# Performance work log

Hardware: AMD Instinct MI355X
Metric: run time of the kernel (lower is better)

Reference implementation:

```python
import jax, jax.numpy as jnp
import numpy as np

B = 4; IN_CH = 256; HEAD_CH = 64; NUM_CLS = 3; H = 128; W = 128
NH = 4; KEY = 16; VAL = 16; OUT_CH = 2
VX = 0.1 * 8; VY = 0.1 * 8  # voxel_size[:2] * out_size_factor
DW = 1.6; DL = 3.9; STRIDE = 1
C_CTR = (HEAD_CH + 2 + NUM_CLS) * 9      # 621
C_COR = (HEAD_CH + 2 + NUM_CLS * 4) * 8  # 624
C_FG = (HEAD_CH + 2 + NUM_CLS) * 9       # 621


def _sampler_points():
    offs = np.arange(-STRIDE, STRIDE + 1, STRIDE, dtype=np.float32)
    oy, ox = np.meshgrid(offs, offs, indexing='ij')
    ctr = np.stack([ox, oy], 0).reshape(2, 9)  # pixel offsets
    cx = np.array([-DW/2, -DW/2, DW/2, DW/2, DL/2, -DL/2, DL/2, -DL/2], np.float32) / VX
    cy = np.array([DL/2, -DL/2, DL/2, -DL/2, -DW/2, -DW/2, DW/2, DW/2], np.float32) / VY
    # faithful to torch: stack(dim=1) -> [8,2] then .view(2,8) (row-major reinterpret)
    cor = np.stack([cx, cy], 1).reshape(2, 8)
    r = max(DW, DL)
    fx = np.array([-r/3, -r/3, -r/3, 0, 0, 0, r/3, r/3, r/3], np.float32) / VX
    fy = np.array([-r/3, 0, r/3, -r/3, 0, r/3, -r/3, 0, r/3], np.float32) / VY
    fg = np.stack([fx, fy], 1).reshape(2, 9)
    return jnp.asarray(ctr), jnp.asarray(cor), jnp.asarray(fg)


def _raw_grid():
    gx = jnp.arange(W, dtype=jnp.float32) + 0.5
    gy = jnp.arange(H, dtype=jnp.float32) + 0.5
    return jnp.stack([jnp.broadcast_to(gx[None, :], (H, W)),
                      jnp.broadcast_to(gy[:, None], (H, W))], 0)  # [2,H,W]


def _conv3x3(x, w, b):
    y = jax.lax.conv_general_dilated(x, w, (1, 1), 'SAME',
                                     dimension_numbers=('NCHW', 'OIHW', 'NCHW'))
    return y + b[None, :, None, None]


def _cbr3(x, w, b, s, t):  # conv3x3 + inference-mode BN (folded scale/shift) + relu
    return jax.nn.relu(_conv3x3(x, w, b) * s[None, :, None, None] + t[None, :, None, None])


def _cbr1(x, w, b, s, t):  # per-head 1x1 conv + BN + relu, w: [NH,O,C], x: [B,C,H,W]
    y = jnp.einsum('noc,bchw->nbohw', w, x) + b[:, None, :, None, None]
    return jax.nn.relu(y * s[:, None, :, None, None] + t[:, None, :, None, None])


def _sample(feats, grids):
    # feats [B,C,H,W]; grids [2,n,H,W] pixel coords. Matches F.grid_sample
    # (bilinear, zeros padding, align_corners=False): sample at pixel coord g-0.5.
    n = grids.shape[1]
    geo = jnp.stack([grids[0] / W, grids[1] / H], 0)  # recover_coords, [2,n,H,W]
    gx, gy = grids[0] - 0.5, grids[1] - 0.5
    x0f = jnp.floor(gx); y0f = jnp.floor(gy)
    dx, dy = gx - x0f, gy - y0f
    x0 = x0f.astype(jnp.int32); y0 = y0f.astype(jnp.int32)
    flat = feats.reshape(B, -1, H * W)

    def gather(xc, yc, wgt):
        valid = ((xc >= 0) & (xc < W) & (yc >= 0) & (yc < H)).astype(feats.dtype) * wgt
        idx = jnp.clip(yc, 0, H - 1) * W + jnp.clip(xc, 0, W - 1)
        v = jnp.take(flat, idx.reshape(-1), axis=2).reshape(B, -1, n, H, W)
        return v * valid[None, None]

    s = (gather(x0, y0, (1 - dx) * (1 - dy)) + gather(x0 + 1, y0, dx * (1 - dy))
         + gather(x0, y0 + 1, (1 - dx) * dy) + gather(x0 + 1, y0 + 1, dx * dy))
    geo_b = jnp.broadcast_to(geo[None], (B,) + geo.shape)
    out = jnp.concatenate([s, geo_b], axis=1)  # [B,C+2,n,H,W]
    return out.reshape(B, -1, H, W)           # channel index = c*n + p, as torch .view


def _forward(base_feats, cc_w, cc_b, cc_s, cc_t, ch_w, ch_b,
             oc_w, oc_b, oc_s, oc_t, oh_w, oh_b,
             fc_w, fc_b, fc_s, fc_t, fh_w, fh_b,
             q_w, q_b, q_s, q_t,
             ck_w, ck_b, ck_s, ck_t, cv_w, cv_b, cv_s, cv_t,
             kk_w, kk_b, kk_s, kk_t, kv_w, kv_b, kv_s, kv_t,
             fk_w, fk_b, fk_s, fk_t, fv_w, fv_b, fv_s, fv_t,
             p1_w, p1_b, p1_s, p1_t, p2_w, p2_b):
    center_feat = _cbr3(base_feats, cc_w, cc_b, cc_s, cc_t)
    center_map = _conv3x3(center_feat, ch_w, ch_b)
    corner_feat = _cbr3(base_feats, oc_w, oc_b, oc_s, oc_t)
    corner_map = _conv3x3(corner_feat, oh_w, oh_b)
    fg_feat = _cbr3(base_feats, fc_w, fc_b, fc_s, fc_t)
    fg_map = _conv3x3(fg_feat, fh_w, fh_b)

    ctr_pts, cor_pts, fg_pts = _sampler_points()
    raw = _raw_grid()
    g_ctr = raw[:, None] + ctr_pts[:, :, None, None]  # [2,9,H,W]
    g_cor = raw[:, None] + cor_pts[:, :, None, None]  # [2,8,H,W]
    g_fg = raw[:, None] + fg_pts[:, :, None, None]    # [2,9,H,W]

    cs = _sample(jnp.concatenate([center_feat, center_map], 1), g_ctr)  # [B,621,H,W]
    os_ = _sample(jnp.concatenate([corner_feat, corner_map], 1), g_cor)  # [B,624,H,W]
    fs = _sample(jnp.concatenate([fg_feat, fg_map], 1), g_fg)            # [B,621,H,W]

    q = _cbr1(base_feats, q_w, q_b, q_s, q_t)  # [NH,B,KEY,H,W]
    ck = _cbr1(cs, ck_w, ck_b, ck_s, ck_t); cv = _cbr1(cs, cv_w, cv_b, cv_s, cv_t)
    ok = _cbr1(os_, kk_w, kk_b, kk_s, kk_t); ov = _cbr1(os_, kv_w, kv_b, kv_s, kv_t)
    fk = _cbr1(fs, fk_w, fk_b, fk_s, fk_t); fv = _cbr1(fs, fv_w, fv_b, fv_s, fv_t)

    logits = jnp.stack([(q * ck).sum(2), (q * ok).sum(2), (q * fk).sum(2)], axis=2)  # [NH,B,3,H,W]
    attw = jax.nn.softmax(logits, axis=2)
    vals = jnp.stack([cv, ov, fv], axis=2)          # [NH,B,3,VAL,H,W]
    att = (attw[:, :, :, None] * vals).sum(2)       # [NH,B,VAL,H,W]

    # predict: 1x1 conv over cat([base_feats, att]) + BN + relu, then 1x1 to out_ch
    h1 = (jnp.einsum('noc,bchw->nbohw', p1_w[:, :, :IN_CH], base_feats)
          + jnp.einsum('nov,nbvhw->nbohw', p1_w[:, :, IN_CH:], att)
          + p1_b[:, None, :, None, None])
    h1 = jax.nn.relu(h1 * p1_s[:, None, :, None, None] + p1_t[:, None, :, None, None])
    pred = jnp.einsum('npo,nbohw->nbphw', p2_w, h1) + p2_b[:, None, :, None, None]
    heads = jnp.moveaxis(pred, 0, 1).reshape(B, NH * OUT_CH, H, W)
    return jnp.concatenate([center_map, corner_map, fg_map, heads], axis=1)  # [B,26,H,W]


def setup_inputs() -> dict:
    ks = iter(jax.random.split(jax.random.key(0), 80))

    def rn(shape, s=0.05):
        return jax.random.normal(next(ks), shape, jnp.float32) * s

    d = {"base_feats": jax.random.normal(next(ks), (B, IN_CH, H, W), jnp.float32)}
    for conv, head, hc in (("cc", "ch", NUM_CLS), ("oc", "oh", NUM_CLS * 4), ("fc", "fh", NUM_CLS)):
        d[conv + "_w"] = rn((HEAD_CH, IN_CH, 3, 3)); d[conv + "_b"] = rn((HEAD_CH,))
        d[conv + "_s"] = 1.0 + rn((HEAD_CH,)); d[conv + "_t"] = rn((HEAD_CH,))
        d[head + "_w"] = rn((hc, HEAD_CH, 3, 3)); d[head + "_b"] = jnp.full((hc,), -2.19, jnp.float32)
    d["q_w"] = rn((NH, KEY, IN_CH)); d["q_b"] = rn((NH, KEY))
    d["q_s"] = 1.0 + rn((NH, KEY)); d["q_t"] = rn((NH, KEY))
    for name, cin, cout in (("ck", C_CTR, KEY), ("cv", C_CTR, VAL), ("kk", C_COR, KEY),
                            ("kv", C_COR, VAL), ("fk", C_FG, KEY), ("fv", C_FG, VAL)):
        d[name + "_w"] = rn((NH, cout, cin)); d[name + "_b"] = rn((NH, cout))
        d[name + "_s"] = 1.0 + rn((NH, cout)); d[name + "_t"] = rn((NH, cout))
    d["p1_w"] = rn((NH, HEAD_CH, IN_CH + VAL)); d["p1_b"] = rn((NH, HEAD_CH))
    d["p1_s"] = 1.0 + rn((NH, HEAD_CH)); d["p1_t"] = rn((NH, HEAD_CH))
    d["p2_w"] = rn((NH, OUT_CH, HEAD_CH)); d["p2_b"] = jnp.full((NH, OUT_CH), -2.19, jnp.float32)
    return d


def reference(base_feats, cc_w, cc_b, cc_s, cc_t, ch_w, ch_b,
              oc_w, oc_b, oc_s, oc_t, oh_w, oh_b,
              fc_w, fc_b, fc_s, fc_t, fh_w, fh_b,
              q_w, q_b, q_s, q_t,
              ck_w, ck_b, ck_s, ck_t, cv_w, cv_b, cv_s, cv_t,
              kk_w, kk_b, kk_s, kk_t, kv_w, kv_b, kv_s, kv_t,
              fk_w, fk_b, fk_s, fk_t, fv_w, fv_b, fv_s, fv_t,
              p1_w, p1_b, p1_s, p1_t, p2_w, p2_b):
    return _forward(base_feats, cc_w, cc_b, cc_s, cc_t, ch_w, ch_b,
                    oc_w, oc_b, oc_s, oc_t, oh_w, oh_b,
                    fc_w, fc_b, fc_s, fc_t, fh_w, fh_b,
                    q_w, q_b, q_s, q_t,
                    ck_w, ck_b, ck_s, ck_t, cv_w, cv_b, cv_s, cv_t,
                    kk_w, kk_b, kk_s, kk_t, kv_w, kv_b, kv_s, kv_t,
                    fk_w, fk_b, fk_s, fk_t, fv_w, fv_b, fv_s, fv_t,
                    p1_w, p1_b, p1_s, p1_t, p2_w, p2_b)
```

## Files before the change

### kernel.cpp

```cpp
#include <hip/hip_runtime.h>
#include <hip/hip_bf16.h>
#include <math.h>


#define HW 16384
#define WIMG 128

typedef unsigned short ushortT;
typedef __attribute__((ext_vector_type(8))) short short8;
typedef __attribute__((ext_vector_type(4))) float floatx4;

constexpr size_t OFF_KV    = 16777216;
constexpr size_t OFF_A16   = 29360128;
constexpr size_t OFF_B16   = 38012928;
constexpr size_t OFF_CWT   = 46057216;
constexpr size_t OFF_CB    = OFF_CWT + 442368;
constexpr size_t OFF_HWT   = OFF_CB + 192;
constexpr size_t OFF_QWT   = OFF_HWT + 20736;
constexpr size_t OFF_QB    = OFF_QWT + 16384;
constexpr size_t OFF_KVW   = OFF_QB + 64;
constexpr size_t OFF_GEO   = OFF_KVW + 241664;
constexpr size_t OFF_P1WT  = OFF_GEO + 1152;
constexpr size_t OFF_P1B   = OFF_P1WT + 81920;

struct P53 { const float* p[53]; };

__device__ inline ushortT f2bf(float f) {
    unsigned u = __float_as_uint(f);
    unsigned r = (u + 0x7FFFu + ((u >> 16) & 1u)) >> 16;
    return (ushortT)r;
}
__device__ inline unsigned packbf(float a, float b) {
    return (unsigned)f2bf(a) | ((unsigned)f2bf(b) << 16);
}
__device__ inline float bf2f(ushortT u) {
    return __uint_as_float((unsigned)u << 16);
}

__device__ const float c_ox[3][9] = {
    {-1.f, 0.f, 1.f, -1.f, 0.f, 1.f, -1.f, 0.f, 1.f},
    {-1.f, 2.4375f, -1.f, -2.4375f, 1.f, 2.4375f, 1.f, -2.4375f, 0.f},
    {-1.625f, -1.625f, -1.625f, 0.f, -1.625f, 1.625f, 0.f, -1.625f, 0.f}};
__device__ const float c_oy[3][9] = {
    {-1.f, -1.f, -1.f, 0.f, 0.f, 0.f, 1.f, 1.f, 1.f},
    {2.4375f, -1.f, -2.4375f, -1.f, 2.4375f, 1.f, -2.4375f, 1.f, 0.f},
    {0.f, 0.f, 1.625f, 1.625f, -1.625f, 1.625f, 0.f, 1.625f, 1.625f}};

__device__ const int tapX_cor[16] = {-1,-1, 2, 3,-1,-1,-3,-2, 1, 1, 2, 3, 1, 1,-3,-2};
__device__ const int tapY_cor[16] = { 2, 3,-1,-1,-3,-2,-1,-1, 2, 3, 1, 1,-3,-2, 1, 1};
__device__ const int tapR_cor[16] = { 4, 5, 2, 2, 0, 1, 2, 2, 4, 5, 3, 3, 0, 1, 3, 3};

__device__ inline float cornw(float off, int X) {
    float f = floorf(off);
    float d = off - f;
    int fi = (int)f;
    return (X == fi) ? (1.f - d) : (X == fi + 1) ? d : 0.f;
}

__global__ __launch_bounds__(256) void prep_kernel(P53 ptrs, float* __restrict__ ws) {
    int i = blockIdx.x * 256 + threadIdx.x;
    const float* const* p = ptrs.p;
    if (i < 442368) {
        int tap = i / 49152, r = i % 49152;
        int g = r / 1536, r2 = r % 1536;
        int M = r2 >> 3, j = r2 & 7;
        int br = M >> 6, oc = M & 63, ic = g * 8 + j;
        float v = p[1 + 6 * br][(oc * 256 + ic) * 9 + tap] * p[3 + 6 * br][oc];
        ((ushortT*)(ws + OFF_CWT))[i] = f2bf(v);
        return;
    }
    i -= 442368;
    if (i < 192) {
        int br = i >> 6, oc = i & 63;
        ws[OFF_CB + i] = p[2 + 6 * br][oc] * p[3 + 6 * br][oc] + p[4 + 6 * br][oc];
        return;
    }
    i -= 192;
    if (i < 27648) {
        int j = i & 7, m = (i >> 3) & 15, u = (i >> 7) % 72, br = i / 9216;
        int cnt = (br == 1) ? 12 : 3;
        int t = u >> 3, g = u & 7, ic = g * 8 + j;
        const float* hw = (br == 0) ? p[5] : (br == 1) ? p[11] : p[17];
        float v = (m < cnt) ? hw[(m * 64 + ic) * 9 + t] : 0.f;
        ((ushortT*)(ws + OFF_HWT))[i] = f2bf(v);
        return;
    }
    i -= 27648;
    if (i < 16384) {
        int j = i & 7, m = (i >> 3) & 63, sg = i >> 9;
        int k = (sg >> 2) * 32 + (sg & 3) * 8 + j;
        ((ushortT*)(ws + OFF_QWT))[i] = f2bf(p[19][m * 256 + k] * p[21][m]);
        return;
    }
    i -= 16384;
    if (i < 64) { ws[OFF_QB + i] = p[20][i] * p[21][i] + p[22][i]; return; }
    i -= 64;
    if (i < 483328) {
        int j = i & 7, m = (i >> 3) & 127, ug = i >> 10;
        int br, NG, NT, n, C, chb, ul;
        if (ug < 84)       { br = 0; NG = 9; NT = 9;  n = 9; C = 67; chb = 0;  ul = ug; }
        else if (ug < 164) { br = 1; NG = 5; NT = 16; n = 8; C = 76; chb = 0;  ul = ug - 84; }
        else if (ug < 244) { br = 1; NG = 5; NT = 16; n = 8; C = 76; chb = 40; ul = ug - 164; }
        else               { br = 2; NG = 9; NT = 25; n = 9; C = 67; chb = 0;  ul = ug - 244; }
        int t = ul / NG, g = ul % NG;
        int c = chb + g * 8 + j;
        float v = 0.f;
        if (t < NT && c < C) {
            int X, Y;
            if (br == 0)      { X = t % 3 - 1; Y = t / 3 - 1; }
            else if (br == 1) { X = tapX_cor[t]; Y = tapY_cor[t]; }
            else              { X = t % 5 - 2; Y = t / 5 - 2; }
            const float* wsrc = (m < 64) ? p[23 + 8 * br] : p[27 + 8 * br];
            int mo = (m < 64) ? m : m - 64;
            float sc = (m < 64) ? p[25 + 8 * br][mo] : p[29 + 8 * br][mo];
            int Cn = (C + 2) * n;
            float s = 0.f;
            for (int pp = 0; pp < n; ++pp) {
                float ww = cornw(c_ox[br][pp], X) * cornw(c_oy[br][pp], Y);
                if (ww != 0.f) s += ww * wsrc[mo * Cn + c * n + pp];
            }
            v = s * sc;
        }
        ((ushortT*)(ws + OFF_KVW))[i] = f2bf(v);
        return;
    }
    i -= 483328;
    if (i < 1152) {
        int br = i / 384, rem = i % 384, which = rem >> 7, m = rem & 127;
        int n = (br == 1) ? 8 : 9, C = (br == 1) ? 76 : 67, Cn = (C + 2) * n;
        const float* wsrc = (m < 64) ? p[23 + 8 * br] : p[27 + 8 * br];
        int mo = (m < 64) ? m : m - 64;
        float sc = (m < 64) ? p[25 + 8 * br][mo] : p[29 + 8 * br][mo];
        float bb = (m < 64) ? p[24 + 8 * br][mo] : p[28 + 8 * br][mo];
        float tt = (m < 64) ? p[26 + 8 * br][mo] : p[30 + 8 * br][mo];
        float v = 0.f;
        if (which == 0) {
            for (int pp = 0; pp < n; ++pp) v += wsrc[mo * Cn + C * n + pp];
            v *= sc;
        } else if (which == 1) {
            for (int pp = 0; pp < n; ++pp) v += wsrc[mo * Cn + (C + 1) * n + pp];
            v *= sc;
        } else {
            for (int pp = 0; pp < n; ++pp)
                v += wsrc[mo * Cn + C * n + pp] * c_ox[br][pp]
                   + wsrc[mo * Cn + (C + 1) * n + pp] * c_oy[br][pp];
            v = v * sc * 0.0078125f + bb * sc + tt;
        }
        ws[OFF_GEO + br * 384 + which * 128 + m] = v;
        return;
    }
    i -= 1152;
    if (i < 81920) {
        int j = i & 7, M = (i >> 3) & 255, sg = i >> 11;
        int k = (sg >> 2) * 32 + (sg & 3) * 8 + j;
        int nh = M >> 6, oc = M & 63;
        float sc = p[49][nh * 64 + oc];
        float v;
        if (k < 256) v = p[47][(nh * 64 + oc) * 272 + k] * sc;
        else {
            int k2 = k - 256, nh2 = k2 >> 4, va = k2 & 15;
            v = (nh2 == nh) ? p[47][(nh * 64 + oc) * 272 + 256 + va] * sc : 0.f;
        }
        ((ushortT*)(ws + OFF_P1WT))[i] = f2bf(v);
        return;
    }
    i -= 81920;
    if (i < 256) { ws[OFF_P1B + i] = p[48][i] * p[49][i] + p[50][i]; return; }
}

__global__ __launch_bounds__(256) void pass_ab(const float* __restrict__ base,
                                               ushortT* __restrict__ a16,
                                               ushortT* __restrict__ b16) {
    int idx = blockIdx.x * 256 + threadIdx.x;
    if (idx < 4 * 32 * 130 * 130) {
        int col = idx % 130, t = idx / 130;
        int row = t % 130; t /= 130;
        int icg = t & 31, b = t >> 5;
        int h = row - 1, w = col - 1;
        unsigned wds[4] = {0u, 0u, 0u, 0u};
        if ((unsigned)h < 128u && (unsigned)w < 128u) {
            const float* s = base + (size_t)(b * 256 + icg * 8) * HW + h * WIMG + w;
            #pragma unroll
            for (int jp = 0; jp < 4; ++jp)
                wds[jp] = packbf(s[(size_t)(2 * jp) * HW], s[(size_t)(2 * jp + 1) * HW]);
        }
        unsigned* d = (unsigned*)(a16 + (size_t)idx * 8);
        d[0] = wds[0]; d[1] = wds[1]; d[2] = wds[2]; d[3] = wds[3];
        return;
    }
    idx -= 4 * 32 * 130 * 130;
    if (idx < 4 * 28 * 134 * 134) {
        int col = idx % 134, row = (idx / 134) % 134;
        if (row < 3 || row >= 131 || col < 3 || col >= 131) {
            unsigned* d = (unsigned*)(b16 + (size_t)idx * 8);
            d[0] = 0u; d[1] = 0u; d[2] = 0u; d[3] = 0u;
        }
    }
}

__global__ __launch_bounds__(256) void conv_base_mfma(
    const ushortT* __restrict__ a16, const ushortT* __restrict__ wA,
    const float* __restrict__ cb, ushortT* __restrict__ b16)
{
    const int wv = threadIdx.x >> 6, lane = threadIdx.x & 63;
    const int sub = lane >> 4, ln = lane & 15;
    const int xh = blockIdx.x, h = blockIdx.y, b = blockIdx.z;
    const int x0 = xh * 64;
    __shared__ __align__(16) ushortT sbuf[8 * 3 * 66 * 8];

    floatx4 acc[3][4];
    #pragma unroll
    for (int mt = 0; mt < 3; ++mt)
        #pragma unroll
        for (int nt = 0; nt < 4; ++nt)
            #pragma unroll
            for (int r = 0; r < 4; ++r) acc[mt][nt][r] = 0.f;

    short8 pf[7];
    auto do_loads = [&](int s) {
        #pragma unroll
        for (int it = 0; it < 7; ++it) {
            int idx = threadIdx.x + it * 256;
            if (idx < 1584) {
                int col = idx % 66, t2 = idx / 66;
                int r = t2 % 3, icg = t2 / 3;
                pf[it] = *(const short8*)(a16 +
                    (((size_t)(b * 32 + s * 8 + icg) * 130 + (h + r)) * 130 + (x0 + col)) * 8);
            }
        }
    };
    do_loads(0);
    #pragma unroll
    for (int s = 0; s < 4; ++s) {
        __syncthreads();
        #pragma unroll
        for (int it = 0; it < 7; ++it) {
            int idx = threadIdx.x + it * 256;
            if (idx < 1584) *(short8*)(sbuf + (size_t)idx * 8) = pf[it];
        }
        __syncthreads();
        if (s < 3) do_loads(s + 1);
        #pragma unroll
        for (int tap = 0; tap < 9; ++tap) {
            const int ky = tap / 3, kx = tap % 3;
            #pragma unroll
            for (int icc = 0; icc < 2; ++icc) {
                const int icgl = icc * 4 + sub;
                short8 Bf[4];
                #pragma unroll
                for (int nt = 0; nt < 4; ++nt) {
                    int c = nt * 16 + ln + kx;
                    Bf[nt] = *(const short8*)(sbuf + ((icgl * 3 + ky) * 66 + c) * 8);
                }
                const int g = s * 8 + icc * 4 + sub;
                short8 Af[3];
                #pragma unroll
                for (int mt = 0; mt < 3; ++mt) {
                    int m = wv * 48 + mt * 16 + ln;
                    Af[mt] = *(const short8*)(wA + (((size_t)tap * 32 + g) * 192 + m) * 8);
                }
                #pragma unroll
                for (int mt = 0; mt < 3; ++mt)
                    #pragma unroll
                    for (int nt = 0; nt < 4; ++nt)
                        acc[mt][nt] = __builtin_amdgcn_mfma_f32_16x16x32_bf16(
                            Af[mt], Bf[nt], acc[mt][nt], 0, 0, 0);
            }
        }
    }
    #pragma unroll
    for (int mt = 0; mt < 3; ++mt)
        #pragma unroll
        for (int nt = 0; nt < 4; ++nt) {
            int px = x0 + nt * 16 + ln;
            int ocq = wv * 48 + mt * 16 + sub * 4;
            float v0 = fmaxf(acc[mt][nt][0] + cb[ocq + 0], 0.f);
            float v1 = fmaxf(acc[mt][nt][1] + cb[ocq + 1], 0.f);
            float v2 = fmaxf(acc[mt][nt][2] + cb[ocq + 2], 0.f);
            float v3 = fmaxf(acc[mt][nt][3] + cb[ocq + 3], 0.f);
            int br = ocq >> 6, oc = ocq & 63;
            int grp = ((br == 0) ? 0 : (br == 1) ? 9 : 19) + (oc >> 3);
            int j0 = oc & 7;
            unsigned* d = (unsigned*)(b16 +
                (((size_t)(b * 28 + grp) * 134 + (h + 3)) * 134 + (px + 3)) * 8 + j0);
            d[0] = packbf(v0, v1); d[1] = packbf(v2, v3);
        }
}

__global__ __launch_bounds__(256) void conv_head_mfma(
    const ushortT* __restrict__ b16c, const ushortT* __restrict__ wH,
    const float* __restrict__ chb, const float* __restrict__ ohb,
    const float* __restrict__ fhb, float* __restrict__ out,
    ushortT* __restrict__ b16)
{
    const int wv = threadIdx.x >> 6, lane = threadIdx.x & 63;
    const int sub = lane >> 4, ln = lane & 15;
    const int h = blockIdx.x;
    const int br = blockIdx.y % 3, b = blockIdx.y / 3;
    const int cnt = (br == 1) ? 12 : 3;
    const int mapb = (br == 0) ? 0 : (br == 1) ? 3 : 15;
    const int grpb = (br == 0) ? 0 : (br == 1) ? 9 : 19;
    const float* bias = (br == 0) ? chb : (br == 1) ? ohb : fhb;
    __shared__ __align__(16) ushortT sbuf[8 * 3 * 130 * 8];

    for (int it = 0; it < 13; ++it) {
        int idx = threadIdx.x + it * 256;
        if (idx < 3120) {
            int col = idx % 130, t2 = idx / 130;
            int r = t2 % 3, g = t2 / 3;
            *(short8*)(sbuf + (size_t)idx * 8) = *(const short8*)(b16c +
                (((size_t)(b * 28 + grpb + g) * 134 + (h + r + 2)) * 134 + (col + 2)) * 8);
        }
    }
    __syncthreads();

    floatx4 acc[2];
    #pragma unroll
    for (int nt = 0; nt < 2; ++nt)
        #pragma unroll
        for (int r = 0; r < 4; ++r) acc[nt][r] = 0.f;
    #pragma unroll
    for (int k = 0; k < 18; ++k) {
        int u = k * 4 + sub;
        int t = u >> 3, g = u & 7;
        int dxv = t % 3 - 1, ry = t / 3;
        short8 Af = *(const short8*)(wH + ((size_t)(br * 72 + u) * 16 + ln) * 8);
        #pragma unroll
        for (int nt = 0; nt < 2; ++nt) {
            int c = wv * 32 + nt * 16 + ln + dxv + 1;
            short8 Bf = *(const short8*)(sbuf + ((g * 3 + ry) * 130 + c) * 8);
            acc[nt] = __builtin_amdgcn_mfma_f32_16x16x32_bf16(Af, Bf, acc[nt], 0, 0, 0);
        }
    }
    #pragma unroll
    for (int nt = 0; nt < 2; ++nt) {
        int px = wv * 32 + nt * 16 + ln;
        #pragma unroll
        for (int r = 0; r < 4; ++r) {
            int m = sub * 4 + r;
            if (m < cnt) {
                float v = acc[nt][r] + bias[m];
                out[((size_t)b * 26 + mapb + m) * HW + h * WIMG + px] = v;
                int grp = grpb + 8 + (m >> 3), j = m & 7;
                b16[(((size_t)(b * 28 + grp) * 134 + (h + 3)) * 134 + (px + 3)) * 8 + j]
                    = f2bf(v);
            }
        }
    }
}

__global__ __launch_bounds__(256) void kv_all(
    const ushortT* __restrict__ b16, const ushortT* __restrict__ kvw,
    const float* __restrict__ geob, ushortT* __restrict__ kvout)
{
    const int lane = threadIdx.x & 63, wv = threadIdx.x >> 6;
    const int sub = lane >> 4, ln = lane & 15;
    const int mw = wv >> 1, nw = wv & 1;
    const int x0 = blockIdx.x * 64, h = blockIdx.y;
    const int brv = blockIdx.z >> 2, b = blockIdx.z & 3;

    const int NGRP = (brv == 1) ? 5 : 9;
    const int NTAP = (brv == 0) ? 9 : (brv == 1) ? 16 : 25;
    const int ROWS = (brv == 0) ? 3 : (brv == 1) ? 6 : 5;
    const int COLS = (brv == 0) ? 66 : (brv == 1) ? 70 : 68;
    const int XMIN = (brv == 0) ? -1 : (brv == 1) ? -3 : -2;
    const int NCHUNK = (brv == 0) ? 21 : (brv == 1) ? 20 : 57;
    const int NPH = (brv == 1) ? 2 : 1;
    const int UBASE = (brv == 0) ? 0 : (brv == 1) ? 9 : 19;
    const ushortT* wU0 = kvw + ((brv == 0) ? 0 : (brv == 1) ? 86016 : 249856);
    const float* geo = geob + brv * 384;

    __shared__ __align__(16) ushortT sbuf[3060 * 8];
    __shared__ int lut[232];

    if (threadIdx.x < 4 * NCHUNK) {
        int u = threadIdx.x;
        unsigned Mng = 0xFFFFFFFFu / (unsigned)NGRP + 1u;
        int t = (int)__umulhi((unsigned)u, Mng);
        int g = u - t * NGRP;
        if (t >= NTAP) t = 0;
        int dxv, ry;
        if (brv == 0)      { dxv = t % 3 - 1; ry = t / 3; }
        else if (brv == 1) { dxv = tapX_cor[t]; ry = tapR_cor[t]; }
        else               { dxv = t % 5 - 2; ry = t / 5; }
        lut[u] = (g * ROWS + ry) * COLS + (dxv - XMIN);
    }

    floatx4 acc[4][2];
    #pragma unroll
    for (int mt = 0; mt < 4; ++mt)
        #pragma unroll
        for (int nt = 0; nt < 2; ++nt)
            #pragma unroll
            for (int r = 0; r < 4; ++r) acc[mt][nt][r] = 0.f;

    const unsigned Mcols = 0xFFFFFFFFu / (unsigned)COLS + 1u;
    const unsigned Mrows = 0xFFFFFFFFu / (unsigned)ROWS + 1u;
    const int NELEM = NGRP * ROWS * COLS;

    for (int ph = 0; ph < NPH; ++ph) {
        const ushortT* wU = wU0 + (size_t)ph * (NCHUNK * 4 * 1024);
        __syncthreads();
        for (int idx = threadIdx.x; idx < NELEM; idx += 256) {
            int row = (int)__umulhi((unsigned)idx, Mcols);
            int col = idx - row * COLS;
            int grp = (int)__umulhi((unsigned)row, Mrows);
            int rw = row - grp * ROWS;
            int dy = (ROWS == 6) ? ((rw < 3) ? rw - 3 : rw - 2) : (rw - (ROWS >> 1));
            *(short8*)(sbuf + (size_t)idx * 8) = *(const short8*)(b16 +
                (((size_t)(b * 28 + UBASE + ph * NGRP + grp) * 134 + (h + dy + 3)) * 134
                 + (x0 + col + XMIN + 3)) * 8);
        }
        __syncthreads();

        short8 A0[4], B0[2], A1[4], B1[2];
        auto ldf = [&](int k, short8 A[4], short8 B[2]) {
            int u = k * 4 + sub;
            int bb = lut[u];
            const ushortT* wp = wU + (size_t)u * 1024;
            #pragma unroll
            for (int mt = 0; mt < 4; ++mt)
                A[mt] = *(const short8*)(wp + (mw * 64 + mt * 16 + ln) * 8);
            #pragma unroll
            for (int nt = 0; nt < 2; ++nt)
                B[nt] = *(const short8*)(sbuf + (size_t)(bb + nw * 32 + nt * 16 + ln) * 8);
        };
        auto dom = [&](short8 A[4], short8 B[2]) {
            #pragma unroll
            for (int mt = 0; mt < 4; ++mt)
                #pragma unroll
                for (int nt = 0; nt < 2; ++nt)
                    acc[mt][nt] = __builtin_amdgcn_mfma_f32_16x16x32_bf16(
                        A[mt], B[nt], acc[mt][nt], 0, 0, 0);
        };
        ldf(0, A0, B0);
        for (int k = 0; k < NCHUNK; k += 2) {
            bool h1 = (k + 1 < NCHUNK);
            if (h1) ldf(k + 1, A1, B1);
            dom(A0, B0);
            if (k + 2 < NCHUNK) ldf(k + 2, A0, B0);
            if (h1) dom(A1, B1);
        }
    }

    const float fy = (h + 0.5f) * 0.0078125f;
    #pragma unroll
    for (int mt = 0; mt < 4; ++mt)
        #pragma unroll
        for (int nt = 0; nt < 2; ++nt) {
            int px = x0 + nw * 32 + nt * 16 + ln;
            float fx = (px + 0.5f) * 0.0078125f;
            #pragma unroll
            for (int r = 0; r < 4; ++r) {
                int Mi = mw * 64 + mt * 16 + sub * 4 + r;
                float v = acc[mt][nt][r] + geo[Mi] * fx + geo[128 + Mi] * fy + geo[256 + Mi];
                kvout[((size_t)(brv * 4 + b) * 128 + Mi) * HW + h * WIMG + px] =
                    f2bf(fmaxf(v, 0.f));
            }
        }
}

__global__ __launch_bounds__(256) void attn_pred_mfma(
    float* __restrict__ ws, const float* __restrict__ p2w,
    const float* __restrict__ p2b, float* __restrict__ out)
{
    const int wv = threadIdx.x >> 6, lane = threadIdx.x & 63;
    const int sub = lane >> 4, ln = lane & 15;
    const int px0 = blockIdx.x * 64, b = blockIdx.y;
    const ushortT* wP1 = (const ushortT*)(ws + OFF_P1WT);
    const ushortT* wQ  = (const ushortT*)(ws + OFF_QWT);
    const ushortT* a16 = (const ushortT*)(ws + OFF_A16);
    const ushortT* kv = (const ushortT*)(ws + OFF_KV);
    const float* p1b = ws + OFF_P1B;
    const float* qb  = ws + OFF_QB;
    __shared__ __align__(16) ushortT xbuf[40 * 64 * 8];
    __shared__ __align__(16) ushortT qld[64 * 64];

    const int mypx = threadIdx.x & 63, nh = threadIdx.x >> 6;
    const int gpx = px0 + mypx, hh = gpx >> 7, ww = gpx & 127;
    #pragma unroll
    for (int g2 = 0; g2 < 8; ++g2) {
        int g = nh * 8 + g2;
        short8 v = *(const short8*)(a16 +
            (((size_t)(b * 32 + g) * 130 + (hh + 1)) * 130 + (ww + 1)) * 8);
        *(short8*)(xbuf + ((size_t)g * 64 + mypx) * 8) = v;
    }
    __syncthreads();

    {
        floatx4 qacc[4];
        #pragma unroll
        for (int nt = 0; nt < 4; ++nt)
            #pragma unroll
            for (int r = 0; r < 4; ++r) qacc[nt][r] = 0.f;
        #pragma unroll
        for (int kk = 0; kk < 8; ++kk) {
            short8 Af = *(const short8*)(wQ + (((kk * 4 + sub) * 64) + wv * 16 + ln) * 8);
            #pragma unroll
            for (int nt = 0; nt < 4; ++nt) {
                short8 Bf = *(const short8*)(xbuf + (((kk * 4 + sub) * 64) + nt * 16 + ln) * 8);
                qacc[nt] = __builtin_amdgcn_mfma_f32_16x16x32_bf16(Af, Bf, qacc[nt], 0, 0, 0);
            }
        }
        #pragma unroll
        for (int nt = 0; nt < 4; ++nt)
            #pragma unroll
            for (int r = 0; r < 4; ++r) {
                int row = wv * 16 + sub * 4 + r;
                qld[row * 64 + nt * 16 + ln] = f2bf(fmaxf(qacc[nt][r] + qb[row], 0.f));
            }
    }
    __syncthreads();

    {
        float l[3];
        #pragma unroll
        for (int br = 0; br < 3; ++br) {
            float s = 0.f;
            #pragma unroll
            for (int ko = 0; ko < 16; ++ko)
                s = fmaf(bf2f(qld[(nh * 16 + ko) * 64 + mypx]),
                         bf2f(kv[(size_t)((br * 4 + b) * 128 + nh * 16 + ko) * HW + gpx]), s);
            l[br] = s;
        }
        float m = fmaxf(l[0], fmaxf(l[1], l[2]));
        float e0 = __expf(l[0] - m), e1 = __expf(l[1] - m), e2 = __expf(l[2] - m);
        float inv = 1.f / (e0 + e1 + e2);
        float aw0 = e0 * inv, aw1 = e1 * inv, aw2 = e2 * inv;
        #pragma unroll
        for (int vap = 0; vap < 8; ++vap) {
            int va0 = vap * 2, va1 = vap * 2 + 1;
            float a0 =
                aw0 * bf2f(kv[(size_t)((0 * 4 + b) * 128 + 64 + nh * 16 + va0) * HW + gpx]) +
                aw1 * bf2f(kv[(size_t)((1 * 4 + b) * 128 + 64 + nh * 16 + va0) * HW + gpx]) +
                aw2 * bf2f(kv[(size_t)((2 * 4 + b) * 128 + 64 + nh * 16 + va0) * HW + gpx]);
            float a1 =
                aw0 * bf2f(kv[(size_t)((0 * 4 + b) * 128 + 64 + nh * 16 + va1) * HW + gpx]) +
                aw1 * bf2f(kv[(size_t)((1 * 4 + b) * 128 + 64 + nh * 16 + va1) * HW + gpx]) +
                aw2 * bf2f(kv[(size_t)((2 * 4 + b) * 128 + 64 + nh * 16 + va1) * HW + gpx]);
            int g = 32 + nh * 2 + (vap >> 2), wo = vap & 3;
            ((unsigned*)xbuf)[(g * 64 + mypx) * 4 + wo] = packbf(a0, a1);
        }
    }
    __syncthreads();

    floatx4 acc[4][4];
    #pragma unroll
    for (int mt = 0; mt < 4; ++mt)
        #pragma unroll
        for (int nt = 0; nt < 4; ++nt)
            #pragma unroll
            for (int r = 0; r < 4; ++r) acc[mt][nt][r] = 0.f;
    #pragma unroll
    for (int kk = 0; kk < 10; ++kk) {
        short8 Bf[4];
        #pragma unroll
        for (int nt = 0; nt < 4; ++nt)
            Bf[nt] = *(const short8*)(xbuf + (((kk * 4 + sub) * 64) + nt * 16 + ln) * 8);
        #pragma unroll
        for (int mt = 0; mt < 4; ++mt) {
            short8 Af = *(const short8*)(wP1 +
                (((size_t)(kk * 4 + sub) * 256) + wv * 64 + mt * 16 + ln) * 8);
            #pragma unroll
            for (int nt = 0; nt < 4; ++nt)
                acc[mt][nt] = __builtin_amdgcn_mfma_f32_16x16x32_bf16(Af, Bf[nt], acc[mt][nt], 0, 0, 0);
        }
    }

    float po0[4] = {0.f, 0.f, 0.f, 0.f}, po1[4] = {0.f, 0.f, 0.f, 0.f};
    #pragma unroll
    for (int mt = 0; mt < 4; ++mt)
        #pragma unroll
        for (int r = 0; r < 4; ++r) {
            int oc = mt * 16 + sub * 4 + r;
            float bias = p1b[wv * 64 + oc];
            float w0 = p2w[(wv * 2 + 0) * 64 + oc];
            float w1 = p2w[(wv * 2 + 1) * 64 + oc];
            #pragma unroll
            for (int nt = 0; nt < 4; ++nt) {
                float hv = fmaxf(acc[mt][nt][r] + bias, 0.f);
                po0[nt] = fmaf(w0, hv, po0[nt]);
                po1[nt] = fmaf(w1, hv, po1[nt]);
            }
        }
    #pragma unroll
    for (int nt = 0; nt < 4; ++nt) {
        po0[nt] += __shfl_xor(po0[nt], 16);
        po0[nt] += __shfl_xor(po0[nt], 32);
        po1[nt] += __shfl_xor(po1[nt], 16);
        po1[nt] += __shfl_xor(po1[nt], 32);
    }
    if (sub == 0) {
        #pragma unroll
        for (int nt = 0; nt < 4; ++nt) {
            int px = px0 + nt * 16 + ln;
            out[((size_t)b * 26 + 18 + wv * 2 + 0) * HW + px] = po0[nt] + p2b[wv * 2 + 0];
            out[((size_t)b * 26 + 18 + wv * 2 + 1) * HW + px] = po1[nt] + p2b[wv * 2 + 1];
        }
    }
}

extern "C" void kernel_launch(void* const* d_in, const int* in_sizes, int n_in,
                              void* d_out, int out_size, void* d_ws, size_t ws_size,
                              hipStream_t stream) {
    (void)in_sizes; (void)n_in; (void)out_size; (void)ws_size;
    float* ws  = (float*)d_ws;
    float* out = (float*)d_out;
    const float* base = (const float*)d_in[0];
    P53 ptrs;
    for (int i = 0; i < 53; ++i) ptrs.p[i] = (const float*)d_in[i];

    ushortT* a16 = (ushortT*)(ws + OFF_A16);
    ushortT* b16 = (ushortT*)(ws + OFF_B16);
    ushortT* kvb = (ushortT*)(ws + OFF_KV);

    prep_kernel<<<4115, 256, 0, stream>>>(ptrs, ws);
    pass_ab<<<16306, 256, 0, stream>>>(base, a16, b16);
    conv_base_mfma<<<dim3(2, 128, 4), 256, 0, stream>>>(
        a16, (const ushortT*)(ws + OFF_CWT), ws + OFF_CB, b16);
    conv_head_mfma<<<dim3(128, 12), 256, 0, stream>>>(
        b16, (const ushortT*)(ws + OFF_HWT),
        (const float*)d_in[6], (const float*)d_in[12], (const float*)d_in[18],
        out, b16);
    kv_all<<<dim3(2, 128, 12), 256, 0, stream>>>(
        b16, (const ushortT*)(ws + OFF_KVW), ws + OFF_GEO, kvb);
    attn_pred_mfma<<<dim3(256, 4), 256, 0, stream>>>(ws, (const float*)d_in[51],
                                                     (const float*)d_in[52], out);
}
```

Baseline: 446.7 us.

## Use direct global-to-LDS loads with double buffering in conv kernels

Replaces register-staged global loads plus LDS stores with global_load_lds (16-byte direct-to-LDS) across the base conv, head conv, sampler and attention kernels. The base conv is restructured into 8 double-buffered stages of 4 channel groups, dropping one barrier per stage. Its epilogue also uses a lane shuffle so each pixel writes one 16-byte store instead of two 8-byte stores. This aims to cut VGPR pressure and LDS write instructions. It relies on the direct-LDS addressing (wave base plus lane*16) matching the previous contiguous layout, and there is no explicit vmcnt wait before the barriers.

```diff
diff --git a/kernel.cpp b/kernel.cpp
--- a/kernel.cpp
+++ b/kernel.cpp
@@ -9,6 +9,7 @@
 typedef unsigned short ushortT;
 typedef __attribute__((ext_vector_type(8))) short short8;
 typedef __attribute__((ext_vector_type(4))) float floatx4;
+typedef __attribute__((ext_vector_type(4))) unsigned uintx4;
 
 constexpr size_t OFF_KV    = 16777216;
 constexpr size_t OFF_A16   = 29360128;
@@ -35,6 +36,12 @@
 }
 __device__ inline float bf2f(ushortT u) {
     return __uint_as_float((unsigned)u << 16);
+}
+
+typedef __attribute__((address_space(3))) ushortT lds_us;
+typedef __attribute__((address_space(1))) const ushortT glb_us;
+__device__ inline void gload_lds16(const ushortT* g, ushortT* ldsbase) {
+    __builtin_amdgcn_global_load_lds((glb_us*)g, (lds_us*)ldsbase, 16, 0, 0);
 }
 
 __device__ const float c_ox[3][9] = {
@@ -206,7 +213,7 @@
     const int sub = lane >> 4, ln = lane & 15;
     const int xh = blockIdx.x, h = blockIdx.y, b = blockIdx.z;
     const int x0 = xh * 64;
-    __shared__ __align__(16) ushortT sbuf[8 * 3 * 66 * 8];
+    __shared__ __align__(16) ushortT sbuf[2][792 * 8];
 
     floatx4 acc[3][4];
     #pragma unroll
@@ -216,75 +223,71 @@
             #pragma unroll
             for (int r = 0; r < 4; ++r) acc[mt][nt][r] = 0.f;
 
-    short8 pf[7];
-    auto do_loads = [&](int s) {
-        #pragma unroll
-        for (int it = 0; it < 7; ++it) {
+    const int wbase = threadIdx.x & ~63;
+    auto stage = [&](int s, int buf) {
+        #pragma unroll
+        for (int it = 0; it < 4; ++it) {
             int idx = threadIdx.x + it * 256;
-            if (idx < 1584) {
+            if (idx < 792) {
                 int col = idx % 66, t2 = idx / 66;
                 int r = t2 % 3, icg = t2 / 3;
-                pf[it] = *(const short8*)(a16 +
-                    (((size_t)(b * 32 + s * 8 + icg) * 130 + (h + r)) * 130 + (x0 + col)) * 8);
+                const ushortT* g = a16 +
+                    (((size_t)(b * 32 + s * 4 + icg) * 130 + (h + r)) * 130 + (x0 + col)) * 8;
+                gload_lds16(g, &sbuf[buf][(size_t)(it * 256 + wbase) * 8]);
             }
         }
     };
-    do_loads(0);
-    #pragma unroll
-    for (int s = 0; s < 4; ++s) {
+    stage(0, 0);
+    for (int s = 0; s < 8; ++s) {
         __syncthreads();
-        #pragma unroll
-        for (int it = 0; it < 7; ++it) {
-            int idx = threadIdx.x + it * 256;
-            if (idx < 1584) *(short8*)(sbuf + (size_t)idx * 8) = pf[it];
-        }
-        __syncthreads();
-        if (s < 3) do_loads(s + 1);
+        if (s < 7) stage(s + 1, (s + 1) & 1);
+        const ushortT* sb = sbuf[s & 1];
         #pragma unroll
         for (int tap = 0; tap < 9; ++tap) {
             const int ky = tap / 3, kx = tap % 3;
-            #pragma unroll
-            for (int icc = 0; icc < 2; ++icc) {
-                const int icgl = icc * 4 + sub;
-                short8 Bf[4];
+            short8 Bf[4];
+            #pragma unroll
+            for (int nt = 0; nt < 4; ++nt) {
+                int c = nt * 16 + ln + kx;
+                Bf[nt] = *(const short8*)(sb + ((sub * 3 + ky) * 66 + c) * 8);
+            }
+            const int g = s * 4 + sub;
+            short8 Af[3];
+            #pragma unroll
+            for (int mt = 0; mt < 3; ++mt) {
+                int m = wv * 48 + mt * 16 + ln;
+                Af[mt] = *(const short8*)(wA + (((size_t)tap * 32 + g) * 192 + m) * 8);
+            }
+            #pragma unroll
+            for (int mt = 0; mt < 3; ++mt)
                 #pragma unroll
-                for (int nt = 0; nt < 4; ++nt) {
-                    int c = nt * 16 + ln + kx;
-                    Bf[nt] = *(const short8*)(sbuf + ((icgl * 3 + ky) * 66 + c) * 8);
-                }
-                const int g = s * 8 + icc * 4 + sub;
-                short8 Af[3];
-                #pragma unroll
-                for (int mt = 0; mt < 3; ++mt) {
-                    int m = wv * 48 + mt * 16 + ln;
-                    Af[mt] = *(const short8*)(wA + (((size_t)tap * 32 + g) * 192 + m) * 8);
-                }
-                #pragma unroll
-                for (int mt = 0; mt < 3; ++mt)
-                    #pragma unroll
-                    for (int nt = 0; nt < 4; ++nt)
-                        acc[mt][nt] = __builtin_amdgcn_mfma_f32_16x16x32_bf16(
-                            Af[mt], Bf[nt], acc[mt][nt], 0, 0, 0);
-            }
-        }
-    }
-    #pragma unroll
-    for (int mt = 0; mt < 3; ++mt)
+                for (int nt = 0; nt < 4; ++nt)
+                    acc[mt][nt] = __builtin_amdgcn_mfma_f32_16x16x32_bf16(
+                        Af[mt], Bf[nt], acc[mt][nt], 0, 0, 0);
+        }
+    }
+    #pragma unroll
+    for (int mt = 0; mt < 3; ++mt) {
+        int ocq = wv * 48 + mt * 16 + sub * 4;
         #pragma unroll
         for (int nt = 0; nt < 4; ++nt) {
             int px = x0 + nt * 16 + ln;
-            int ocq = wv * 48 + mt * 16 + sub * 4;
             float v0 = fmaxf(acc[mt][nt][0] + cb[ocq + 0], 0.f);
             float v1 = fmaxf(acc[mt][nt][1] + cb[ocq + 1], 0.f);
             float v2 = fmaxf(acc[mt][nt][2] + cb[ocq + 2], 0.f);
             float v3 = fmaxf(acc[mt][nt][3] + cb[ocq + 3], 0.f);
-            int br = ocq >> 6, oc = ocq & 63;
-            int grp = ((br == 0) ? 0 : (br == 1) ? 9 : 19) + (oc >> 3);
-            int j0 = oc & 7;
-            unsigned* d = (unsigned*)(b16 +
-                (((size_t)(b * 28 + grp) * 134 + (h + 3)) * 134 + (px + 3)) * 8 + j0);
-            d[0] = packbf(v0, v1); d[1] = packbf(v2, v3);
-        }
+            unsigned lo = packbf(v0, v1), hi = packbf(v2, v3);
+            unsigned plo = (unsigned)__shfl_down((int)lo, 16);
+            unsigned phi = (unsigned)__shfl_down((int)hi, 16);
+            if (!(sub & 1)) {
+                int br = ocq >> 6, oc = ocq & 63;
+                int grp = ((br == 0) ? 0 : (br == 1) ? 9 : 19) + (oc >> 3);
+                uintx4 w = {lo, hi, plo, phi};
+                *(uintx4*)(b16 +
+                    (((size_t)(b * 28 + grp) * 134 + (h + 3)) * 134 + (px + 3)) * 8) = w;
+            }
+        }
+    }
 }
 
 __global__ __launch_bounds__(256) void conv_head_mfma(
@@ -302,14 +305,16 @@
     const int grpb = (br == 0) ? 0 : (br == 1) ? 9 : 19;
     const float* bias = (br == 0) ? chb : (br == 1) ? ohb : fhb;
     __shared__ __align__(16) ushortT sbuf[8 * 3 * 130 * 8];
+    const int wbase = threadIdx.x & ~63;
 
     for (int it = 0; it < 13; ++it) {
         int idx = threadIdx.x + it * 256;
         if (idx < 3120) {
             int col = idx % 130, t2 = idx / 130;
             int r = t2 % 3, g = t2 / 3;
-            *(short8*)(sbuf + (size_t)idx * 8) = *(const short8*)(b16c +
-                (((size_t)(b * 28 + grpb + g) * 134 + (h + r + 2)) * 134 + (col + 2)) * 8);
+            const ushortT* gp = b16c +
+                (((size_t)(b * 28 + grpb + g) * 134 + (h + r + 2)) * 134 + (col + 2)) * 8;
+            gload_lds16(gp, sbuf + (size_t)(it * 256 + wbase) * 8);
         }
     }
     __syncthreads();
@@ -372,6 +377,7 @@
 
     __shared__ __align__(16) ushortT sbuf[3060 * 8];
     __shared__ int lut[232];
+    const int wbase = threadIdx.x & ~63;
 
     if (threadIdx.x < 4 * NCHUNK) {
         int u = threadIdx.x;
@@ -397,19 +403,24 @@
     const unsigned Mcols = 0xFFFFFFFFu / (unsigned)COLS + 1u;
     const unsigned Mrows = 0xFFFFFFFFu / (unsigned)ROWS + 1u;
     const int NELEM = NGRP * ROWS * COLS;
+    const int NITER = (NELEM + 255) >> 8;
 
     for (int ph = 0; ph < NPH; ++ph) {
         const ushortT* wU = wU0 + (size_t)ph * (NCHUNK * 4 * 1024);
         __syncthreads();
-        for (int idx = threadIdx.x; idx < NELEM; idx += 256) {
-            int row = (int)__umulhi((unsigned)idx, Mcols);
-            int col = idx - row * COLS;
-            int grp = (int)__umulhi((unsigned)row, Mrows);
-            int rw = row - grp * ROWS;
-            int dy = (ROWS == 6) ? ((rw < 3) ? rw - 3 : rw - 2) : (rw - (ROWS >> 1));
-            *(short8*)(sbuf + (size_t)idx * 8) = *(const short8*)(b16 +
-                (((size_t)(b * 28 + UBASE + ph * NGRP + grp) * 134 + (h + dy + 3)) * 134
-                 + (x0 + col + XMIN + 3)) * 8);
+        for (int it = 0; it < NITER; ++it) {
+            int idx = threadIdx.x + it * 256;
+            if (idx < NELEM) {
+                int row = (int)__umulhi((unsigned)idx, Mcols);
+                int col = idx - row * COLS;
+                int grp = (int)__umulhi((unsigned)row, Mrows);
+                int rw = row - grp * ROWS;
+                int dy = (ROWS == 6) ? ((rw < 3) ? rw - 3 : rw - 2) : (rw - (ROWS >> 1));
+                const ushortT* gp = b16 +
+                    (((size_t)(b * 28 + UBASE + ph * NGRP + grp) * 134 + (h + dy + 3)) * 134
+                     + (x0 + col + XMIN + 3)) * 8;
+                gload_lds16(gp, sbuf + (size_t)(it * 256 + wbase) * 8);
+            }
         }
         __syncthreads();
 
@@ -481,9 +492,9 @@
     #pragma unroll
     for (int g2 = 0; g2 < 8; ++g2) {
         int g = nh * 8 + g2;
-        short8 v = *(const short8*)(a16 +
-            (((size_t)(b * 32 + g) * 130 + (hh + 1)) * 130 + (ww + 1)) * 8);
-        *(short8*)(xbuf + ((size_t)g * 64 + mypx) * 8) = v;
+        const ushortT* gp = a16 +
+            (((size_t)(b * 32 + g) * 130 + (hh + 1)) * 130 + (ww + 1)) * 8;
+        gload_lds16(gp, xbuf + (size_t)g * 64 * 8);
     }
     __syncthreads();
 
```

Result: faster. 435.4 us (-2.5%).
